# Optimization experiments

Measured on AMD Instinct MI355X. Metric: run time of the kernel, lower is better.

## Reference

```python
import jax, jax.numpy as jnp
import numpy as np

N_NODES = 100000


def gcn_conv(x, src, dst, W, b):
    # x: [N, F_in]; src/dst: [E'] (self-loops already appended)
    n = x.shape[0]
    deg = jax.ops.segment_sum(jnp.ones_like(src, dtype=x.dtype), dst, num_segments=n)
    dinv = jnp.where(deg > 0, jax.lax.rsqrt(deg), 0.0)
    norm = dinv[src] * dinv[dst]                      # [E']
    h = x @ W                                         # [N, F_out] (GEMM first: F_out small)
    msg = h[src] * norm[:, None]                      # gather + scale
    out = jax.ops.segment_sum(msg, dst, num_segments=n)  # scatter-add
    return out + b


def setup_inputs() -> dict:
    key = jax.random.key(0)
    k1, k2, k3, k4 = jax.random.split(key, 4)
    x = jax.random.normal(k1, (N_NODES, 1433), dtype=jnp.float32)
    edge_index = jax.random.randint(k2, (2, 3200000), 0, N_NODES, dtype=jnp.int32)
    W1 = jax.random.normal(k3, (1433, 32), dtype=jnp.float32) * (1.0 / np.sqrt(1433.0))
    b1 = jnp.zeros((32,), dtype=jnp.float32)
    W2 = jax.random.normal(k4, (32, 7), dtype=jnp.float32) * (1.0 / np.sqrt(32.0))
    b2 = jnp.zeros((7,), dtype=jnp.float32)
    return {"x": x, "edge_index": edge_index, "W1": W1, "b1": b1, "W2": W2, "b2": b2}


def reference(x, edge_index, W1, b1, W2, b2):
    n = x.shape[0]
    loop = jnp.arange(n, dtype=edge_index.dtype)      # add self-loops (GCNConv default)
    src = jnp.concatenate([edge_index[0], loop])
    dst = jnp.concatenate([edge_index[1], loop])
    h = gcn_conv(x, src, dst, W1, b1)
    h = jax.nn.relu(h)
    # F.dropout with training=False (eval mode) is identity
    h = gcn_conv(h, src, dst, W2, b2)
    return jax.nn.log_softmax(h, axis=1)
```

## Files before the change

kernel.cpp:

```cpp
#include <hip/hip_runtime.h>
#include <math.h>

#define F0 1433
#define F1 32
#define F2 7

__global__ void k_init_deg(float* __restrict__ deg, int N) {
    int i = blockIdx.x * 256 + threadIdx.x;
    if (i < N) deg[i] = 1.0f;
}

__global__ void k_count_deg(const int* __restrict__ dst, float* __restrict__ deg, int E) {
    int e = blockIdx.x * 256 + threadIdx.x;
    if (e < E) atomicAdd(&deg[dst[e]], 1.0f);
}

__global__ void k_dinv(float* __restrict__ deg, int N) {
    int i = blockIdx.x * 256 + threadIdx.x;
    if (i < N) deg[i] = rsqrtf(deg[i]);
}

#define BM 128
#define BK 64
#define NT_FULL 22
#define KTAIL 1408

typedef const __attribute__((address_space(1))) void* gas_ptr;
typedef __attribute__((address_space(3))) void* las_ptr;

__device__ __forceinline__ void gl_lds4(const void* g, void* l) {
    __builtin_amdgcn_global_load_lds((gas_ptr)g, (las_ptr)l, 4, 0, 0);
}

#define COMPUTE()                                                            \
    _Pragma("unroll")                                                        \
    for (int kk = 0; kk < BK; kk += 4) {                                     \
        const int xo = (((kk >> 2) ^ key) << 2);                             \
        float4 x0 = *(const float4*)&xs[(r     ) * BK + xo];                 \
        float4 x1 = *(const float4*)&xs[(r + 32) * BK + xo];                 \
        float4 x2 = *(const float4*)&xs[(r + 64) * BK + xo];                 \
        float4 x3 = *(const float4*)&xs[(r + 96) * BK + xo];                 \
        const float a0[4] = {x0.x, x0.y, x0.z, x0.w};                        \
        const float a1[4] = {x1.x, x1.y, x1.z, x1.w};                        \
        const float a2[4] = {x2.x, x2.y, x2.z, x2.w};                        \
        const float a3[4] = {x3.x, x3.y, x3.z, x3.w};                        \
        _Pragma("unroll")                                                    \
        for (int u = 0; u < 4; ++u) {                                        \
            float4 w = *(const float4*)&wsm[(kk + u) * F1 + cg * 4];         \
            acc[0][0] += a0[u] * w.x; acc[0][1] += a0[u] * w.y;              \
            acc[0][2] += a0[u] * w.z; acc[0][3] += a0[u] * w.w;              \
            acc[1][0] += a1[u] * w.x; acc[1][1] += a1[u] * w.y;              \
            acc[1][2] += a1[u] * w.z; acc[1][3] += a1[u] * w.w;              \
            acc[2][0] += a2[u] * w.x; acc[2][1] += a2[u] * w.y;              \
            acc[2][2] += a2[u] * w.z; acc[2][3] += a2[u] * w.w;              \
            acc[3][0] += a3[u] * w.x; acc[3][1] += a3[u] * w.y;              \
            acc[3][2] += a3[u] * w.z; acc[3][3] += a3[u] * w.w;              \
        }                                                                    \
    }

__global__ __launch_bounds__(256) void k_gemm1(const float* __restrict__ x,
                                               const float* __restrict__ W,
                                               const float* __restrict__ dinv,
                                               float* __restrict__ h,
                                               float* __restrict__ agg, int N) {
    __shared__ float xs[BM * BK];
    __shared__ float wsm[BK * F1];
    const int tid  = threadIdx.x;
    const int lane = tid & 63;
    const int wv   = tid >> 6;
    const int row0 = blockIdx.x * BM;
    const int cg   = tid & 7;
    const int r    = tid >> 3;
    const int key  = r & 7;
    const bool rowfull = (row0 + BM <= N);

    int lo[8];
    #pragma unroll
    for (int q = 0; q < 8; ++q)
        lo[q] = (((lane >> 2) ^ q) << 2) | (lane & 3);

    float acc[4][4] = {{0.f, 0.f, 0.f, 0.f}, {0.f, 0.f, 0.f, 0.f},
                       {0.f, 0.f, 0.f, 0.f}, {0.f, 0.f, 0.f, 0.f}};

    for (int t = 0; t < NT_FULL; ++t) {
        const int k0 = t * BK;
        __syncthreads();
        if (rowfull) {
            const float* xb = x + (size_t)(row0 + wv * 32) * F0 + k0;
            #pragma unroll
            for (int it = 0; it < 32; ++it)
                gl_lds4(xb + (size_t)it * F0 + lo[it & 7],
                        xs + (wv * 32 + it) * BK);
        } else {
            #pragma unroll
            for (int it = 0; it < 32; ++it) {
                int gr = row0 + wv * 32 + it;
                if (gr > N - 1) gr = N - 1;
                gl_lds4(x + (size_t)gr * F0 + k0 + lo[it & 7],
                        xs + (wv * 32 + it) * BK);
            }
        }
        {
            const float* wb = W + (size_t)k0 * F1 + wv * 512 + lane;
            #pragma unroll
            for (int it = 0; it < 8; ++it)
                gl_lds4(wb + it * 64, wsm + wv * 512 + it * 64);
        }
        __syncthreads();
        COMPUTE();
    }

    __syncthreads();
    {
        const int j = lane;
        const int i0 = wv;
        #pragma unroll
        for (int l = 0; l < 32; ++l) {
            int row = i0 + 4 * l;
            int gr = row0 + row;
            int gk = KTAIL + j;
            float v = (gr < N && gk < F0) ? x[(size_t)gr * F0 + gk] : 0.f;
            xs[row * BK + ((((j >> 2) ^ (row & 7)) << 2) | (j & 3))] = v;
        }
        #pragma unroll
        for (int l = 0; l < 8; ++l) {
            int idx = tid + l * 256;
            int gk = KTAIL + (idx >> 5);
            wsm[idx] = (gk < F0) ? W[gk * F1 + (idx & 31)] : 0.f;
        }
    }
    __syncthreads();
    COMPUTE();

    #pragma unroll
    for (int m = 0; m < 4; ++m) {
        int gr = row0 + r + 32 * m;
        if (gr < N) {
            float4 o = make_float4(acc[m][0], acc[m][1], acc[m][2], acc[m][3]);
            *(float4*)&h[(size_t)gr * F1 + cg * 4] = o;
            float d = dinv[gr];
            float dd = d * d;
            *(float4*)&agg[(size_t)gr * F1 + cg * 4] =
                make_float4(o.x * dd, o.y * dd, o.z * dd, o.w * dd);
        }
    }
}

__global__ void k_scatter1(const int* __restrict__ src, const int* __restrict__ dst,
                           const float* __restrict__ dinv, const float* __restrict__ h1,
                           float* __restrict__ agg, int E) {
    int t = blockIdx.x * 256 + threadIdx.x;
    int e = t >> 5;
    if (e >= E) return;
    int f = t & 31;
    int s = src[e], d = dst[e];
    float w = dinv[s] * dinv[d];
    atomicAdd(&agg[d * F1 + f], h1[s * F1 + f] * w);
}

__global__ __launch_bounds__(256) void k_layer2(const float* __restrict__ agg1,
                                                const float* __restrict__ b1,
                                                const float* __restrict__ W2,
                                                const float* __restrict__ dinv,
                                                float* __restrict__ h2,
                                                float* __restrict__ out, int N) {
    __shared__ float w2s[F1 * F2];
    __shared__ float b1s[F1];
    int tid = threadIdx.x;
    if (tid < F1 * F2) w2s[tid] = W2[tid];
    if (tid < F1) b1s[tid] = b1[tid];
    __syncthreads();
    int i = blockIdx.x * 256 + tid;
    if (i >= N) return;
    float v[F1];
    #pragma unroll
    for (int u = 0; u < 8; ++u) {
        float4 t = *(const float4*)&agg1[(long)i * F1 + u * 4];
        v[u*4+0] = fmaxf(t.x + b1s[u*4+0], 0.f);
        v[u*4+1] = fmaxf(t.y + b1s[u*4+1], 0.f);
        v[u*4+2] = fmaxf(t.z + b1s[u*4+2], 0.f);
        v[u*4+3] = fmaxf(t.w + b1s[u*4+3], 0.f);
    }
    float o[F2] = {0.f, 0.f, 0.f, 0.f, 0.f, 0.f, 0.f};
    #pragma unroll
    for (int k = 0; k < F1; ++k) {
        float a = v[k];
        #pragma unroll
        for (int c = 0; c < F2; ++c) o[c] += a * w2s[k * F2 + c];
    }
    float di = dinv[i];
    float dd = di * di;
    #pragma unroll
    for (int c = 0; c < F2; ++c) {
        h2[(long)i * F2 + c] = o[c];
        out[(long)i * F2 + c] = o[c] * dd;
    }
}

__global__ void k_scatter2(const int* __restrict__ src, const int* __restrict__ dst,
                           const float* __restrict__ dinv, const float* __restrict__ h2,
                           float* __restrict__ out, int E) {
    int t = blockIdx.x * 256 + threadIdx.x;
    int e = t >> 3;
    int c = t & 7;
    if (e >= E || c >= F2) return;
    int s = src[e], d = dst[e];
    float w = dinv[s] * dinv[d];
    atomicAdd(&out[(long)d * F2 + c], h2[(long)s * F2 + c] * w);
}

__global__ void k_logsoftmax(float* __restrict__ out, const float* __restrict__ b2, int N) {
    int i = blockIdx.x * 256 + threadIdx.x;
    if (i >= N) return;
    float v[F2];
    float m = -1e30f;
    #pragma unroll
    for (int c = 0; c < F2; ++c) {
        v[c] = out[(long)i * F2 + c] + b2[c];
        m = fmaxf(m, v[c]);
    }
    float s = 0.f;
    #pragma unroll
    for (int c = 0; c < F2; ++c) s += expf(v[c] - m);
    float l = logf(s);
    #pragma unroll
    for (int c = 0; c < F2; ++c) out[(long)i * F2 + c] = v[c] - m - l;
}

extern "C" void kernel_launch(void* const* d_in, const int* in_sizes, int n_in,
                              void* d_out, int out_size, void* d_ws, size_t ws_size,
                              hipStream_t stream) {
    const float* x  = (const float*)d_in[0];
    const int*   ei = (const int*)d_in[1];
    const float* W1 = (const float*)d_in[2];
    const float* b1 = (const float*)d_in[3];
    const float* W2 = (const float*)d_in[4];
    const float* b2 = (const float*)d_in[5];
    float* out = (float*)d_out;

    const int N = in_sizes[0] / F0;
    const int E = in_sizes[1] / 2;
    const int* src = ei;
    const int* dst = ei + E;

    float* ws   = (float*)d_ws;
    size_t o    = 0;
    float* dinv = ws;        o += (size_t)((N + 3) & ~3);
    float* h1   = ws + o;    o += (size_t)N * F1;
    float* agg1 = ws + o;    o += (size_t)N * F1;
    float* h2   = h1;

    const int nb_N  = (N + 255) / 256;
    const int nb_E  = (E + 255) / 256;

    k_init_deg  <<<nb_N, 256, 0, stream>>>(dinv, N);
    k_count_deg <<<nb_E, 256, 0, stream>>>(dst, dinv, E);
    k_dinv      <<<nb_N, 256, 0, stream>>>(dinv, N);

    k_gemm1     <<<(N + BM - 1) / BM, 256, 0, stream>>>(x, W1, dinv, h1, agg1, N);

    k_scatter1  <<<((size_t)E * 32 + 255) / 256, 256, 0, stream>>>(src, dst, dinv, h1, agg1, E);

    k_layer2    <<<nb_N, 256, 0, stream>>>(agg1, b1, W2, dinv, h2, out, N);

    k_scatter2  <<<((size_t)E * 8 + 255) / 256, 256, 0, stream>>>(src, dst, dinv, h2, out, E);

    k_logsoftmax<<<nb_N, 256, 0, stream>>>(out, b2, N);
}
```

Baseline: 1.669 ms.

## Double-buffer GEMM1 LDS tiles so async loads overlap compute

The first-layer GEMM now keeps two LDS buffers and halves the K tile size. The global-to-LDS DMA for the next tile is issued before computing the current one, which removes one barrier per iteration and hides load latency behind FMA work. W tiles are loaded with 16-byte global_load_lds instead of 4-byte ones. The partial-block branch is replaced by clamping the row-chunk base, which only stays correct when the out-of-range rows are never stored.

Result: slower. 1.768 ms (+5.9%).

```diff
diff --git a/kernel.cpp b/kernel.cpp
--- a/kernel.cpp
+++ b/kernel.cpp
@@ -21,8 +21,8 @@
 }
 
 #define BM 128
-#define BK 64
-#define NT_FULL 22
+#define BK 32
+#define NT_FULL 44
 #define KTAIL 1408
 
 typedef const __attribute__((address_space(1))) void* gas_ptr;
@@ -31,22 +31,35 @@
 __device__ __forceinline__ void gl_lds4(const void* g, void* l) {
     __builtin_amdgcn_global_load_lds((gas_ptr)g, (las_ptr)l, 4, 0, 0);
 }
-
-#define COMPUTE()                                                            \
+__device__ __forceinline__ void gl_lds16(const void* g, void* l) {
+    __builtin_amdgcn_global_load_lds((gas_ptr)g, (las_ptr)l, 16, 0, 0);
+}
+
+#define STAGE_DMA(B)                                                         \
+    {                                                                        \
+        _Pragma("unroll")                                                    \
+        for (int it = 0; it < 16; ++it) {                                    \
+            const float* p = xb + (size_t)((it >> 2) * (8 * F0)) + offm[it & 3]; \
+            gl_lds4(p, &xs[B][(wv * 32 + it * 2) * BK]);                     \
+        }                                                                    \
+        gl_lds16(wb, &wsm[B][wv * 256]);                                     \
+    }
+
+#define COMPUTE(B)                                                           \
     _Pragma("unroll")                                                        \
     for (int kk = 0; kk < BK; kk += 4) {                                     \
         const int xo = (((kk >> 2) ^ key) << 2);                             \
-        float4 x0 = *(const float4*)&xs[(r     ) * BK + xo];                 \
-        float4 x1 = *(const float4*)&xs[(r + 32) * BK + xo];                 \
-        float4 x2 = *(const float4*)&xs[(r + 64) * BK + xo];                 \
-        float4 x3 = *(const float4*)&xs[(r + 96) * BK + xo];                 \
+        float4 x0 = *(const float4*)&xs[B][(r     ) * BK + xo];              \
+        float4 x1 = *(const float4*)&xs[B][(r + 32) * BK + xo];              \
+        float4 x2 = *(const float4*)&xs[B][(r + 64) * BK + xo];              \
+        float4 x3 = *(const float4*)&xs[B][(r + 96) * BK + xo];              \
         const float a0[4] = {x0.x, x0.y, x0.z, x0.w};                        \
         const float a1[4] = {x1.x, x1.y, x1.z, x1.w};                        \
         const float a2[4] = {x2.x, x2.y, x2.z, x2.w};                        \
         const float a3[4] = {x3.x, x3.y, x3.z, x3.w};                        \
         _Pragma("unroll")                                                    \
         for (int u = 0; u < 4; ++u) {                                        \
-            float4 w = *(const float4*)&wsm[(kk + u) * F1 + cg * 4];         \
+            float4 w = *(const float4*)&wsm[B][(kk + u) * F1 + cg * 4];      \
             acc[0][0] += a0[u] * w.x; acc[0][1] += a0[u] * w.y;              \
             acc[0][2] += a0[u] * w.z; acc[0][3] += a0[u] * w.w;              \
             acc[1][0] += a1[u] * w.x; acc[1][1] += a1[u] * w.y;              \
@@ -63,8 +76,8 @@
                                                const float* __restrict__ dinv,
                                                float* __restrict__ h,
                                                float* __restrict__ agg, int N) {
-    __shared__ float xs[BM * BK];
-    __shared__ float wsm[BK * F1];
+    __shared__ float xs[2][BM * BK];
+    __shared__ float wsm[2][BK * F1];
     const int tid  = threadIdx.x;
     const int lane = tid & 63;
     const int wv   = tid >> 6;
@@ -72,65 +85,52 @@
     const int cg   = tid & 7;
     const int r    = tid >> 3;
     const int key  = r & 7;
-    const bool rowfull = (row0 + BM <= N);
-
-    int lo[8];
-    #pragma unroll
-    for (int q = 0; q < 8; ++q)
-        lo[q] = (((lane >> 2) ^ q) << 2) | (lane & 3);
+
+    const int srow = lane >> 5;
+    const int scol = lane & 31;
+    int offm[4];
+    #pragma unroll
+    for (int m = 0; m < 4; ++m) {
+        int rk = (2 * m + srow) & 7;
+        offm[m] = (2 * m + srow) * F0 + ((((scol >> 2) ^ rk) << 2) | (scol & 3));
+    }
+    int chunk0 = row0 + wv * 32;
+    if (chunk0 > N - 32) chunk0 = N - 32;
+    const float* xb = x + (size_t)chunk0 * F0;
+    const float* wb = W + wv * 256 + lane * 4;
 
     float acc[4][4] = {{0.f, 0.f, 0.f, 0.f}, {0.f, 0.f, 0.f, 0.f},
                        {0.f, 0.f, 0.f, 0.f}, {0.f, 0.f, 0.f, 0.f}};
 
+    STAGE_DMA(0)
+    xb += BK; wb += BK * F1;
+    __syncthreads();
+
     for (int t = 0; t < NT_FULL; ++t) {
-        const int k0 = t * BK;
+        if (t + 1 < NT_FULL) {
+            STAGE_DMA((t + 1) & 1)
+            xb += BK; wb += BK * F1;
+        }
+        COMPUTE(t & 1)
         __syncthreads();
-        if (rowfull) {
-            const float* xb = x + (size_t)(row0 + wv * 32) * F0 + k0;
-            #pragma unroll
-            for (int it = 0; it < 32; ++it)
-                gl_lds4(xb + (size_t)it * F0 + lo[it & 7],
-                        xs + (wv * 32 + it) * BK);
-        } else {
-            #pragma unroll
-            for (int it = 0; it < 32; ++it) {
-                int gr = row0 + wv * 32 + it;
-                if (gr > N - 1) gr = N - 1;
-                gl_lds4(x + (size_t)gr * F0 + k0 + lo[it & 7],
-                        xs + (wv * 32 + it) * BK);
-            }
-        }
-        {
-            const float* wb = W + (size_t)k0 * F1 + wv * 512 + lane;
-            #pragma unroll
-            for (int it = 0; it < 8; ++it)
-                gl_lds4(wb + it * 64, wsm + wv * 512 + it * 64);
-        }
-        __syncthreads();
-        COMPUTE();
-    }
-
+    }
+
+    #pragma unroll
+    for (int l = 0; l < 16; ++l) {
+        int idx = tid + l * 256;
+        int row = idx >> 5, col = idx & 31;
+        int gr = row0 + row, gk = KTAIL + col;
+        float v = (gr < N && gk < F0) ? x[(size_t)gr * F0 + gk] : 0.f;
+        xs[0][row * BK + ((((col >> 2) ^ (row & 7)) << 2) | (col & 3))] = v;
+    }
+    #pragma unroll
+    for (int l = 0; l < 4; ++l) {
+        int idx = tid + l * 256;
+        int gk = KTAIL + (idx >> 5);
+        wsm[0][idx] = (gk < F0) ? W[(size_t)gk * F1 + (idx & 31)] : 0.f;
+    }
     __syncthreads();
-    {
-        const int j = lane;
-        const int i0 = wv;
-        #pragma unroll
-        for (int l = 0; l < 32; ++l) {
-            int row = i0 + 4 * l;
-            int gr = row0 + row;
-            int gk = KTAIL + j;
-            float v = (gr < N && gk < F0) ? x[(size_t)gr * F0 + gk] : 0.f;
-            xs[row * BK + ((((j >> 2) ^ (row & 7)) << 2) | (j & 3))] = v;
-        }
-        #pragma unroll
-        for (int l = 0; l < 8; ++l) {
-            int idx = tid + l * 256;
-            int gk = KTAIL + (idx >> 5);
-            wsm[idx] = (gk < F0) ? W[gk * F1 + (idx & 31)] : 0.f;
-        }
-    }
-    __syncthreads();
-    COMPUTE();
+    COMPUTE(0)
 
     #pragma unroll
     for (int m = 0; m < 4; ++m) {
```
